# Optimization experiments

Hardware: AMD Instinct MI355X
Metric: run time of the kernel (lower is better)

Reference implementation:

```python
import jax, jax.numpy as jnp
import numpy as np
import math

S, E, D, H = 4096, 512, 64, 8  # sentence_length, imbd_size, hidden_size, num_heads


def setup_inputs() -> dict:
    key = jax.random.key(0)
    k1, k2, k3, k4, k5 = jax.random.split(key, 5)
    return {
        "X": jax.random.normal(k1, (S, E), dtype=jnp.float32),
        "W_q": jax.random.uniform(k2, (H, E, D), dtype=jnp.float32),
        "W_k": jax.random.uniform(k3, (H, E, D), dtype=jnp.float32),
        "W_v": jax.random.uniform(k4, (H, E, D), dtype=jnp.float32),
        "W_0": jax.random.uniform(k5, (E, D), dtype=jnp.float32),
    }


def reference(X, W_q, W_k, W_v, W_0):
    # Per-head projections: X [S,E] broadcast across heads -> [H,S,D]
    q = jnp.einsum('se,hed->hsd', X, W_q)
    k = jnp.einsum('se,hed->hsd', X, W_k)
    v = jnp.einsum('se,hed->hsd', X, W_v)
    # Scaled scores [H,S,S]; softmax over keys (last axis), no mask
    scores = jnp.einsum('hsd,htd->hst', q, k) / math.sqrt(D)
    attn = jax.nn.softmax(scores, axis=-1)
    r3 = jnp.einsum('hst,htd->hsd', attn, v)  # [H,S,D]
    # Concat heads: permute to [S,H,D] -> [S,H*D], then output proj [E,D]
    Z = r3.transpose(1, 0, 2).reshape(S, H * D) @ W_0  # [S,D]
    return Z
```

## Files before the change

kernel.cpp:

```cpp
#include <hip/hip_runtime.h>
#include <hip/hip_bf16.h>

#define S_LEN 4096
#define E_DIM 512
#define D_DIM 64
#define H_NUM 8
#define KSPLIT 4
#define NKT ((S_LEN / KSPLIT) / 64)
#define QSCALE 0.18033688011112042f

typedef short bf16x8 __attribute__((ext_vector_type(8)));
typedef float f32x4 __attribute__((ext_vector_type(4)));
typedef unsigned short u16x8 __attribute__((ext_vector_type(8)));
typedef unsigned short u16x4 __attribute__((ext_vector_type(4)));

__device__ inline unsigned short f2bf(float x) {
    union { float f; unsigned u; } v; v.f = x;
    unsigned r = v.u + 0x7FFFu + ((v.u >> 16) & 1u);
    return (unsigned short)(r >> 16);
}
__device__ inline float bf2f(unsigned short b) {
    union { unsigned u; float f; } v; v.u = ((unsigned)b) << 16;
    return v.f;
}
__device__ inline f32x4 mfma16(bf16x8 a, bf16x8 b, f32x4 c) {
    return __builtin_amdgcn_mfma_f32_16x16x32_bf16(a, b, c, 0, 0, 0);
}
__device__ inline void gl_lds16(const void* g, void* l) {
    __builtin_amdgcn_global_load_lds(
        (const __attribute__((address_space(1))) void*)g,
        (__attribute__((address_space(3))) void*)l, 16, 0, 0);
}
__device__ inline unsigned cvtpk(float a, float b) {
    unsigned r;
    asm volatile("v_cvt_pk_bf16_f32 %0, %1, %2" : "=v"(r) : "v"(a), "v"(b));
    return r;
}

__global__ __launch_bounds__(256) void prepass_kernel(
    const float* __restrict__ X, const float* __restrict__ Wq,
    const float* __restrict__ Wk, const float* __restrict__ Wv,
    unsigned short* __restrict__ Xhi, unsigned short* __restrict__ Xlo,
    unsigned short* __restrict__ WT)
{
    int bx = blockIdx.x;
    if (bx < 2048) {
        int i = (bx * 256 + threadIdx.x) * 4;
        float4 v = *(const float4*)&X[i];
        float a[4] = {v.x, v.y, v.z, v.w};
        u16x4 hv, lv;
#pragma unroll
        for (int j = 0; j < 4; ++j) {
            unsigned short hb = f2bf(a[j]);
            hv[j] = hb;
            lv[j] = f2bf(a[j] - bf2f(hb));
        }
        *(u16x4*)&Xhi[i] = hv;
        *(u16x4*)&Xlo[i] = lv;
    } else {
        int wid = bx - 2048;
        int z = wid >> 8;
        const float* W = (z == 0) ? Wq : (z == 1) ? Wk : Wv;
        int idx = (wid & 255) * 256 + threadIdx.x;
        int n = idx >> 7;
        int e = (idx & 127) * 4;
        int hh = n >> 6, d = n & 63;
        unsigned short* Whi = WT + (size_t)z * 2 * 262144;
        unsigned short* Wlo = Whi + 262144;
        u16x4 hv, lv;
#pragma unroll
        for (int j = 0; j < 4; ++j) {
            float v = W[((size_t)hh * E_DIM + e + j) * D_DIM + d];
            unsigned short hb = f2bf(v);
            hv[j] = hb;
            lv[j] = f2bf(v - bf2f(hb));
        }
        *(u16x4*)&Whi[(size_t)n * E_DIM + e] = hv;
        *(u16x4*)&Wlo[(size_t)n * E_DIM + e] = lv;
    }
}

__global__ __launch_bounds__(256) void proj_kernel(
    const unsigned short* __restrict__ Xhi, const unsigned short* __restrict__ Xlo,
    const unsigned short* __restrict__ WT,
    unsigned short* __restrict__ Qhi, unsigned short* __restrict__ Qlo,
    unsigned short* __restrict__ Khi, unsigned short* __restrict__ Klo,
    unsigned short* __restrict__ Vt)
{
    __shared__ __align__(16) unsigned short XhS[128 * 64];
    __shared__ __align__(16) unsigned short XlS[128 * 64];
    __shared__ __align__(16) unsigned short WhS[128 * 64];
    __shared__ __align__(16) unsigned short WlS[128 * 64];

    const int s0 = blockIdx.x * 128, n0 = blockIdx.y * 128, z = blockIdx.z;
    const unsigned short* Wh_g = WT + (size_t)z * 524288;
    const unsigned short* Wl_g = Wh_g + 262144;

    const int tid = threadIdx.x, lane = tid & 63, w = tid >> 6;
    const int l15 = lane & 15, lhi = lane >> 4;
    const int wr = w >> 1, wc = w & 1;

    const int chunk = lane & 7;
    size_t aoff[4], boff[4];
    int ldso[4];
#pragma unroll
    for (int i = 0; i < 4; ++i) {
        int r = w * 32 + i * 8 + (lane >> 3);
        int swz = (chunk * 16) ^ ((r & 7) << 4);
        aoff[i] = ((size_t)(s0 + r)) * 1024 + swz;
        boff[i] = ((size_t)(n0 + r)) * 1024 + swz;
        ldso[i] = (w * 32 + i * 8) * 128;
    }

    f32x4 acc[4][4];
#pragma unroll
    for (int a = 0; a < 4; ++a)
#pragma unroll
        for (int b = 0; b < 4; ++b) acc[a][b] = (f32x4){0.f, 0.f, 0.f, 0.f};

    for (int kb = 0; kb < E_DIM; kb += 64) {
        __syncthreads();
#pragma unroll
        for (int i = 0; i < 4; ++i) {
            size_t ab = aoff[i] + kb * 2;
            size_t bb = boff[i] + kb * 2;
            gl_lds16((const char*)Xhi + ab, (char*)XhS + ldso[i]);
            gl_lds16((const char*)Xlo + ab, (char*)XlS + ldso[i]);
            gl_lds16((const char*)Wh_g + bb, (char*)WhS + ldso[i]);
            gl_lds16((const char*)Wl_g + bb, (char*)WlS + ldso[i]);
        }
        __syncthreads();

#pragma unroll
        for (int kc = 0; kc < 2; ++kc) {
            int cb = kc * 64 + lhi * 16;
            bf16x8 ah[4], al[4], bh[4], bl[4];
#pragma unroll
            for (int rt = 0; rt < 4; ++rt) {
                int row = wr * 64 + rt * 16 + l15;
                int ad = row * 128 + (cb ^ ((row & 7) << 4));
                ah[rt] = *(const bf16x8*)((const char*)XhS + ad);
                al[rt] = *(const bf16x8*)((const char*)XlS + ad);
            }
#pragma unroll
            for (int nt = 0; nt < 4; ++nt) {
                int n = wc * 64 + nt * 16 + l15;
                int bd = n * 128 + (cb ^ ((n & 7) << 4));
                bh[nt] = *(const bf16x8*)((const char*)WhS + bd);
                bl[nt] = *(const bf16x8*)((const char*)WlS + bd);
            }
#pragma unroll
            for (int rt = 0; rt < 4; ++rt)
#pragma unroll
                for (int nt = 0; nt < 4; ++nt) {
                    acc[rt][nt] = mfma16(ah[rt], bh[nt], acc[rt][nt]);
                    acc[rt][nt] = mfma16(ah[rt], bl[nt], acc[rt][nt]);
                    acc[rt][nt] = mfma16(al[rt], bh[nt], acc[rt][nt]);
                }
        }
    }

#pragma unroll
    for (int rt = 0; rt < 4; ++rt)
#pragma unroll
        for (int nt = 0; nt < 4; ++nt) {
            int n = n0 + wc * 64 + nt * 16 + l15;
            int hh = n >> 6, d = n & 63;
            if (z == 2) {
                u16x4 vv;
#pragma unroll
                for (int j = 0; j < 4; ++j) vv[j] = f2bf(acc[rt][nt][j]);
                int sb = s0 + wr * 64 + rt * 16 + lhi * 4;
                *(u16x4*)&Vt[((size_t)(hh * D_DIM + d)) * S_LEN + sb] = vv;
            } else {
#pragma unroll
                for (int j = 0; j < 4; ++j) {
                    int s = s0 + wr * 64 + rt * 16 + lhi * 4 + j;
                    float val = acc[rt][nt][j];
                    size_t o = ((size_t)hh * S_LEN + s) * D_DIM + d;
                    if (z == 0) {
                        val *= QSCALE;
                        unsigned short hb = f2bf(val);
                        Qhi[o] = hb;
                        Qlo[o] = f2bf(val - bf2f(hb));
                    } else {
                        unsigned short hb = f2bf(val);
                        Khi[o] = hb;
                        Klo[o] = f2bf(val - bf2f(hb));
                    }
                }
            }
        }
}

__global__ __launch_bounds__(256) void flash_kernel(
    const unsigned short* __restrict__ Qhi, const unsigned short* __restrict__ Qlo,
    const unsigned short* __restrict__ Khi_g, const unsigned short* __restrict__ Klo_g,
    const unsigned short* __restrict__ Vt_g,
    unsigned short* __restrict__ Part, float2* __restrict__ ML)
{
    __shared__ __align__(16) char lds[24576];
    __shared__ __align__(16) unsigned short PS[4][2][16 * 64];

    const int h  = blockIdx.y;
    const int ks = blockIdx.z;
    const int q0 = blockIdx.x * 128;
    const int tid  = threadIdx.x;
    const int lane = tid & 63;
    const int w    = tid >> 6;
    const int l15  = lane & 15;
    const int lhi  = lane >> 4;

    bf16x8 qh[2][2], ql[2][2];
#pragma unroll
    for (int g = 0; g < 2; ++g) {
        const int qrow = q0 + g * 64 + w * 16 + l15;
#pragma unroll
        for (int c = 0; c < 2; ++c) {
            size_t off = ((size_t)(h * S_LEN + qrow)) * D_DIM + lhi * 8 + 32 * c;
            qh[g][c] = *(const bf16x8*)&Qhi[off];
            ql[g][c] = *(const bf16x8*)&Qlo[off];
        }
    }

    const char *pKh[2], *pKl[2], *pV[2];
    int ldsd[2];
    {
        const int chunk = lane & 7;
#pragma unroll
        for (int i = 0; i < 2; ++i) {
            int r = w * 16 + i * 8 + (lane >> 3);
            int swz = (chunk * 16) ^ ((r & 7) << 4);
            size_t kb = ((size_t)(h * S_LEN + ks * (S_LEN / KSPLIT) + r)) * 128 + swz;
            pKh[i] = (const char*)Khi_g + kb;
            pKl[i] = (const char*)Klo_g + kb;
            size_t vb = ((size_t)(h * D_DIM + r) * S_LEN + ks * (S_LEN / KSPLIT)) * 2 + swz;
            pV[i] = (const char*)Vt_g + vb;
            ldsd[i] = (w * 16 + i * 8) * 128;
        }
    }

    f32x4 acc_o[2][4];
#pragma unroll
    for (int g = 0; g < 2; ++g)
#pragma unroll
        for (int nt = 0; nt < 4; ++nt) acc_o[g][nt] = (f32x4){0.f, 0.f, 0.f, 0.f};
    float m2[2] = {-1e30f, -1e30f};
    float lsum[2] = {0.f, 0.f};

    for (int kt = 0; kt < NKT; ++kt) {
        __syncthreads();
#pragma unroll
        for (int i = 0; i < 2; ++i) {
            gl_lds16(pKh[i], lds + ldsd[i]);
            gl_lds16(pKl[i], lds + 8192 + ldsd[i]);
            gl_lds16(pV[i],  lds + 16384 + ldsd[i]);
            pKh[i] += 8192; pKl[i] += 8192; pV[i] += 128;
        }
        __syncthreads();

        const char* Kh = lds;
        const char* Kl = lds + 8192;
        const char* Vl = lds + 16384;

        f32x4 sacc[2][4];
#pragma unroll
        for (int g = 0; g < 2; ++g)
#pragma unroll
            for (int nt = 0; nt < 4; ++nt) sacc[g][nt] = (f32x4){0.f, 0.f, 0.f, 0.f};
        __builtin_amdgcn_s_setprio(1);
#pragma unroll
        for (int c = 0; c < 2; ++c) {
            int colb = (lhi * 8 + 32 * c) * 2;
#pragma unroll
            for (int nt = 0; nt < 4; ++nt) {
                int key = l15 + 16 * nt;
                int lo = key * 128 + (((colb >> 4) ^ (key & 7)) << 4);
                bf16x8 kh = *(const bf16x8*)(Kh + lo);
                bf16x8 kl = *(const bf16x8*)(Kl + lo);
#pragma unroll
                for (int g = 0; g < 2; ++g) {
                    sacc[g][nt] = mfma16(kh, qh[g][c], sacc[g][nt]);
                    sacc[g][nt] = mfma16(kl, qh[g][c], sacc[g][nt]);
                    sacc[g][nt] = mfma16(kh, ql[g][c], sacc[g][nt]);
                }
            }
        }
        __builtin_amdgcn_s_setprio(0);

#pragma unroll
        for (int g = 0; g < 2; ++g) {
            float mx0 = fmaxf(fmaxf(sacc[g][0][0], sacc[g][0][1]), fmaxf(sacc[g][0][2], sacc[g][0][3]));
            float mx1 = fmaxf(fmaxf(sacc[g][1][0], sacc[g][1][1]), fmaxf(sacc[g][1][2], sacc[g][1][3]));
            float mx2 = fmaxf(fmaxf(sacc[g][2][0], sacc[g][2][1]), fmaxf(sacc[g][2][2], sacc[g][2][3]));
            float mx3 = fmaxf(fmaxf(sacc[g][3][0], sacc[g][3][1]), fmaxf(sacc[g][3][2], sacc[g][3][3]));
            float vm = fmaxf(fmaxf(mx0, mx1), fmaxf(mx2, mx3));
            vm = fmaxf(vm, __shfl_xor(vm, 16));
            vm = fmaxf(vm, __shfl_xor(vm, 32));

            if (!__all(vm <= m2[g] + 8.f)) {
                float mnew = fmaxf(m2[g], vm);
                float sc = exp2f(m2[g] - mnew);
                m2[g] = mnew;
                lsum[g] *= sc;
                float scj[4];
#pragma unroll
                for (int j = 0; j < 4; ++j) scj[j] = __shfl(sc, lhi * 4 + j);
#pragma unroll
                for (int nt = 0; nt < 4; ++nt)
#pragma unroll
                    for (int j = 0; j < 4; ++j) acc_o[g][nt][j] *= scj[j];
            }

            float sum = 0.f;
            unsigned short* pw = &PS[w][g][0];
#pragma unroll
            for (int nt = 0; nt < 4; ++nt) {
                float e0 = exp2f(sacc[g][nt][0] - m2[g]);
                float e1 = exp2f(sacc[g][nt][1] - m2[g]);
                float e2 = exp2f(sacc[g][nt][2] - m2[g]);
                float e3 = exp2f(sacc[g][nt][3] - m2[g]);
                sum += (e0 + e1) + (e2 + e3);
                int colb = 32 * nt + 8 * lhi;
                int adr = l15 * 128 + ((((colb >> 4)) ^ (l15 & 7)) << 4) + (colb & 15);
                uint2 pk = make_uint2(cvtpk(e0, e1), cvtpk(e2, e3));
                *(uint2*)((char*)pw + adr) = pk;
            }
            sum += __shfl_xor(sum, 16);
            sum += __shfl_xor(sum, 32);
            lsum[g] += sum;
        }

        __builtin_amdgcn_s_setprio(1);
#pragma unroll
        for (int c = 0; c < 2; ++c) {
            int colb = (lhi * 8 + 32 * c) * 2;
            int loA = l15 * 128 + (((colb >> 4) ^ (l15 & 7)) << 4);
            bf16x8 pa0 = *(const bf16x8*)((const char*)&PS[w][0][0] + loA);
            bf16x8 pa1 = *(const bf16x8*)((const char*)&PS[w][1][0] + loA);
#pragma unroll
            for (int nt = 0; nt < 4; ++nt) {
                int d = l15 + 16 * nt;
                int loB = d * 128 + (((colb >> 4) ^ (d & 7)) << 4);
                bf16x8 vb = *(const bf16x8*)(Vl + loB);
                acc_o[0][nt] = mfma16(pa0, vb, acc_o[0][nt]);
                acc_o[1][nt] = mfma16(pa1, vb, acc_o[1][nt]);
            }
        }
        __builtin_amdgcn_s_setprio(0);
    }

    unsigned short* PT = Part + ((size_t)(ks * H_NUM + h)) * S_LEN * D_DIM;
#pragma unroll
    for (int g = 0; g < 2; ++g) {
        if (lane < 16) {
            ML[(size_t)(ks * H_NUM + h) * S_LEN + q0 + g * 64 + w * 16 + l15] =
                make_float2(m2[g], lsum[g]);
        }
#pragma unroll
        for (int r = 0; r < 4; ++r) {
            float lr = __shfl(lsum[g], lhi * 4 + r);
            float inv = 1.f / lr;
            int s = q0 + g * 64 + w * 16 + lhi * 4 + r;
#pragma unroll
            for (int nt = 0; nt < 4; ++nt)
                PT[(size_t)s * D_DIM + l15 + 16 * nt] = f2bf(acc_o[g][nt][r] * inv);
        }
    }
}

__global__ __launch_bounds__(256) void cw_kernel(
    const float2* __restrict__ ML, float4* __restrict__ CW)
{
    int i = blockIdx.x * 256 + threadIdx.x;
    float2 a[KSPLIT];
    float m = -1e30f;
#pragma unroll
    for (int k = 0; k < KSPLIT; ++k) {
        a[k] = ML[(size_t)k * H_NUM * S_LEN + i];
        m = fmaxf(m, a[k].x);
    }
    float wk[KSPLIT], wsum = 0.f;
#pragma unroll
    for (int k = 0; k < KSPLIT; ++k) {
        wk[k] = exp2f(a[k].x - m) * a[k].y;
        wsum += wk[k];
    }
    float inv = 1.f / wsum;
    CW[i] = make_float4(wk[0] * inv, wk[1] * inv, wk[2] * inv, wk[3] * inv);
}

__global__ __launch_bounds__(256) void zout_kernel(
    const unsigned short* __restrict__ Part, const float4* __restrict__ CW,
    const float* __restrict__ W0, float* __restrict__ Z)
{
    __shared__ __align__(16) float Rs[32][64];
    __shared__ __align__(16) float Ws[32][64];

    const size_t PSZ = (size_t)H_NUM * S_LEN * D_DIM;
    const int s0 = blockIdx.x * 64;
    const int tid = threadIdx.x;
    const int tx = tid & 15;
    const int ty = tid >> 4;

    float acc[4][4];
#pragma unroll
    for (int i = 0; i < 4; ++i)
#pragma unroll
        for (int j = 0; j < 4; ++j) acc[i][j] = 0.f;

    for (int kb = 0; kb < E_DIM; kb += 32) {
        __syncthreads();
#pragma unroll
        for (int p = 0; p < 2; ++p) {
            int idx = tid + 256 * p;
            int row = idx >> 3;
            int kq  = idx & 7;
            int k = kb + kq * 4;
            int hh = k >> 6, d0 = k & 63;
            int s = s0 + row;
            size_t pbase = ((size_t)hh * S_LEN + s) * D_DIM + d0;
            float4 c = *(const float4*)&CW[hh * S_LEN + s];
            u16x4 a0 = *(const u16x4*)&Part[pbase];
            u16x4 a1 = *(const u16x4*)&Part[PSZ + pbase];
            u16x4 a2 = *(const u16x4*)&Part[2 * PSZ + pbase];
            u16x4 a3 = *(const u16x4*)&Part[3 * PSZ + pbase];
#pragma unroll
            for (int j = 0; j < 4; ++j)
                Rs[kq * 4 + j][row] = bf2f(a0[j]) * c.x + bf2f(a1[j]) * c.y +
                                      bf2f(a2[j]) * c.z + bf2f(a3[j]) * c.w;
        }
#pragma unroll
        for (int p = 0; p < 2; ++p) {
            int idx = tid + 256 * p;
            int k  = idx >> 4;
            int nq = idx & 15;
            *(float4*)&Ws[k][nq * 4] = *(const float4*)&W0[(size_t)(kb + k) * D_DIM + nq * 4];
        }
        __syncthreads();

#pragma unroll 8
        for (int k = 0; k < 32; ++k) {
            float a[4], b[4];
            *(float4*)&a[0] = *(const float4*)&Rs[k][ty * 4];
            *(float4*)&b[0] = *(const float4*)&Ws[k][tx * 4];
#pragma unroll
            for (int i = 0; i < 4; ++i)
#pragma unroll
                for (int j = 0; j < 4; ++j) acc[i][j] += a[i] * b[j];
        }
    }

#pragma unroll
    for (int i = 0; i < 4; ++i) {
        float4 o = make_float4(acc[i][0], acc[i][1], acc[i][2], acc[i][3]);
        *(float4*)&Z[(size_t)(s0 + ty * 4 + i) * D_DIM + tx * 4] = o;
    }
}

extern "C" void kernel_launch(void* const* d_in, const int* in_sizes, int n_in,
                              void* d_out, int out_size, void* d_ws, size_t ws_size,
                              hipStream_t stream) {
    const float* X  = (const float*)d_in[0];
    const float* Wq = (const float*)d_in[1];
    const float* Wk = (const float*)d_in[2];
    const float* Wv = (const float*)d_in[3];
    const float* W0 = (const float*)d_in[4];

    char* ws = (char*)d_ws;
    const size_t MB = 1ull << 20;
    unsigned short* Qhi = (unsigned short*)(ws + 0 * MB);
    unsigned short* Qlo = (unsigned short*)(ws + 4 * MB);
    unsigned short* Khi = (unsigned short*)(ws + 8 * MB);
    unsigned short* Klo = (unsigned short*)(ws + 12 * MB);
    unsigned short* Vt  = (unsigned short*)(ws + 16 * MB);
    unsigned short* Xhi = (unsigned short*)(ws + 24 * MB);
    unsigned short* Xlo = (unsigned short*)(ws + 28 * MB);
    unsigned short* WT  = (unsigned short*)(ws + 32 * MB);
    unsigned short* Part = (unsigned short*)(ws + 20 * MB);
    float2* ML = (float2*)(ws + 36 * MB);
    float4* CW = (float4*)(ws + 37 * MB);

    float* Z = (float*)d_out;

    prepass_kernel<<<dim3(2048 + 768), 256, 0, stream>>>(X, Wq, Wk, Wv, Xhi, Xlo, WT);
    proj_kernel<<<dim3(S_LEN / 128, 4, 3), 256, 0, stream>>>(
        Xhi, Xlo, WT, Qhi, Qlo, Khi, Klo, Vt);
    flash_kernel<<<dim3(S_LEN / 128, H_NUM, KSPLIT), 256, 0, stream>>>(
        Qhi, Qlo, Khi, Klo, Vt, Part, ML);
    cw_kernel<<<dim3(H_NUM * S_LEN / 256), 256, 0, stream>>>(ML, CW);
    zout_kernel<<<dim3(S_LEN / 64), 256, 0, stream>>>(Part, CW, W0, Z);
}
```

Baseline: 229.2 us.

## Load K/V fragments directly from global memory and remap flash blocks for L2 locality

The flash kernel no longer stages K-hi, K-lo and V tiles into shared memory with two barriers per tile. Each wave now reads its MFMA operand fragments straight from global memory through the cache. A 1D grid with a block-index swizzle is added so that blocks sharing the same head and key split run close together, which should improve L2 reuse. This removes the LDS traffic and the synchronisation, but every wave now fetches the same K/V data redundantly and depends on cache hits to absorb global-memory latency, with no software prefetching.

```diff
diff --git a/kernel.cpp b/kernel.cpp
--- a/kernel.cpp
+++ b/kernel.cpp
@@ -199,12 +199,15 @@
     const unsigned short* __restrict__ Vt_g,
     unsigned short* __restrict__ Part, float2* __restrict__ ML)
 {
-    __shared__ __align__(16) char lds[24576];
     __shared__ __align__(16) unsigned short PS[4][2][16 * 64];
 
-    const int h  = blockIdx.y;
-    const int ks = blockIdx.z;
-    const int q0 = blockIdx.x * 128;
+    const int bid = blockIdx.x;
+    const int swz = (bid & 7) * 128 + (bid >> 3);
+    const int qb = swz & 31;
+    const int h  = (swz >> 5) & 7;
+    const int ks = swz >> 8;
+    const int q0 = qb * 128;
+
     const int tid  = threadIdx.x;
     const int lane = tid & 63;
     const int w    = tid >> 6;
@@ -223,22 +226,11 @@
         }
     }
 
-    const char *pKh[2], *pKl[2], *pV[2];
-    int ldsd[2];
-    {
-        const int chunk = lane & 7;
-#pragma unroll
-        for (int i = 0; i < 2; ++i) {
-            int r = w * 16 + i * 8 + (lane >> 3);
-            int swz = (chunk * 16) ^ ((r & 7) << 4);
-            size_t kb = ((size_t)(h * S_LEN + ks * (S_LEN / KSPLIT) + r)) * 128 + swz;
-            pKh[i] = (const char*)Khi_g + kb;
-            pKl[i] = (const char*)Klo_g + kb;
-            size_t vb = ((size_t)(h * D_DIM + r) * S_LEN + ks * (S_LEN / KSPLIT)) * 2 + swz;
-            pV[i] = (const char*)Vt_g + vb;
-            ldsd[i] = (w * 16 + i * 8) * 128;
-        }
-    }
+    const size_t krow0 = (size_t)(h * S_LEN + ks * (S_LEN / KSPLIT) + l15) * 128 + lhi * 16;
+    const char* KhiB = (const char*)Khi_g + krow0;
+    const char* KloB = (const char*)Klo_g + krow0;
+    const char* VtB = (const char*)Vt_g +
+        (((size_t)(h * D_DIM + l15)) * S_LEN + ks * (S_LEN / KSPLIT) + lhi * 8) * 2;
 
     f32x4 acc_o[2][4];
 #pragma unroll
@@ -249,19 +241,9 @@
     float lsum[2] = {0.f, 0.f};
 
     for (int kt = 0; kt < NKT; ++kt) {
-        __syncthreads();
-#pragma unroll
-        for (int i = 0; i < 2; ++i) {
-            gl_lds16(pKh[i], lds + ldsd[i]);
-            gl_lds16(pKl[i], lds + 8192 + ldsd[i]);
-            gl_lds16(pV[i],  lds + 16384 + ldsd[i]);
-            pKh[i] += 8192; pKl[i] += 8192; pV[i] += 128;
-        }
-        __syncthreads();
-
-        const char* Kh = lds;
-        const char* Kl = lds + 8192;
-        const char* Vl = lds + 16384;
+        const char* Kh = KhiB + kt * 8192;
+        const char* Kl = KloB + kt * 8192;
+        const char* Vv = VtB + kt * 128;
 
         f32x4 sacc[2][4];
 #pragma unroll
@@ -271,13 +253,10 @@
         __builtin_amdgcn_s_setprio(1);
 #pragma unroll
         for (int c = 0; c < 2; ++c) {
-            int colb = (lhi * 8 + 32 * c) * 2;
 #pragma unroll
             for (int nt = 0; nt < 4; ++nt) {
-                int key = l15 + 16 * nt;
-                int lo = key * 128 + (((colb >> 4) ^ (key & 7)) << 4);
-                bf16x8 kh = *(const bf16x8*)(Kh + lo);
-                bf16x8 kl = *(const bf16x8*)(Kl + lo);
+                bf16x8 kh = *(const bf16x8*)(Kh + nt * 2048 + 64 * c);
+                bf16x8 kl = *(const bf16x8*)(Kl + nt * 2048 + 64 * c);
 #pragma unroll
                 for (int g = 0; g < 2; ++g) {
                     sacc[g][nt] = mfma16(kh, qh[g][c], sacc[g][nt]);
@@ -340,9 +319,7 @@
             bf16x8 pa1 = *(const bf16x8*)((const char*)&PS[w][1][0] + loA);
 #pragma unroll
             for (int nt = 0; nt < 4; ++nt) {
-                int d = l15 + 16 * nt;
-                int loB = d * 128 + (((colb >> 4) ^ (d & 7)) << 4);
-                bf16x8 vb = *(const bf16x8*)(Vl + loB);
+                bf16x8 vb = *(const bf16x8*)(Vv + nt * (S_LEN * 2 * 16) + 64 * c);
                 acc_o[0][nt] = mfma16(pa0, vb, acc_o[0][nt]);
                 acc_o[1][nt] = mfma16(pa1, vb, acc_o[1][nt]);
             }
@@ -486,7 +463,7 @@
     prepass_kernel<<<dim3(2048 + 768), 256, 0, stream>>>(X, Wq, Wk, Wv, Xhi, Xlo, WT);
     proj_kernel<<<dim3(S_LEN / 128, 4, 3), 256, 0, stream>>>(
         Xhi, Xlo, WT, Qhi, Qlo, Khi, Klo, Vt);
-    flash_kernel<<<dim3(S_LEN / 128, H_NUM, KSPLIT), 256, 0, stream>>>(
+    flash_kernel<<<dim3(32 * H_NUM * KSPLIT), 256, 0, stream>>>(
         Qhi, Qlo, Khi, Klo, Vt, Part, ML);
     cw_kernel<<<dim3(H_NUM * S_LEN / 256), 256, 0, stream>>>(ML, CW);
     zout_kernel<<<dim3(S_LEN / 64), 256, 0, stream>>>(Part, CW, W0, Z);
```

After: 317.8 us. +38.7%, slower.
